# Optimization experiments

Measured on AMD Instinct MI355X. Metric: run time of the kernel, lower is better.

## Reference

```python
import jax, jax.numpy as jnp
import numpy as np
import itertools

BINS_NUM = 35
BINS_SIZE = 9
ORDERS = (2, 3, 4, 5)

def _comb_idx(n, k):
    # combinations with replacement of indices 0..n-1, shape [ncomb, k]
    return np.array(list(itertools.combinations_with_replacement(range(n), k)), dtype=np.int32)

_COMB = {k: _comb_idx(BINS_SIZE, k) for k in ORDERS}


def setup_inputs() -> dict:
    key = jax.random.key(0)
    x = jax.random.normal(key, (1024, BINS_NUM * BINS_SIZE), dtype=jnp.float32)
    return {"x": x}


def reference(x) -> jnp.ndarray:
    B = x.shape[0]
    bins = x.reshape(B, BINS_NUM, BINS_SIZE)          # [B, 35, 9]
    parts = [bins]                                     # 'origin' slice first
    for k in ORDERS:
        idx = jnp.asarray(_COMB[k])                    # [ncomb_k, k]
        gathered = bins[:, :, idx]                     # [B, 35, ncomb_k, k]
        parts.append(jnp.prod(gathered, axis=-1))      # [B, 35, ncomb_k]
    # per-bin concat [origin, de2, de3, de4, de5], then flatten bins -> matches
    # torch's outer concat over bins since bin is the leading concat axis here.
    out = jnp.concatenate(parts, axis=-1)              # [B, 35, 2001]
    return out.reshape(B, -1)                          # [B, 70035]
```

## Files before the change

### kernel.cpp

```cpp
#include <hip/hip_runtime.h>

#define BSZ 9
#define NPB 2001
#define N2 45
#define N3 165
#define N4 495
#define N5 1287
#define O2 9
#define O3 54
#define O4 219
#define O5 714
#define LSLOTS 714

#define WAVE_SYNC() asm volatile("s_waitcnt lgkmcnt(0)" ::: "memory")

constexpr unsigned pslot2(unsigned i, unsigned j) {
    return O2 + i * 9u - i * (i - 1u) / 2u + (j - i);
}

struct Tabs {
    unsigned short p2[N2];
    unsigned short p3[N3];
    unsigned short p4[N4];
    unsigned short p5[N5];
};
constexpr Tabs make_tabs() {
    Tabs t{};
    { int p = 0;
      for (unsigned i = 0; i < 9; ++i)
          for (unsigned j = i; j < 9; ++j)
              t.p2[p++] = (unsigned short)(i | (j << 8)); }
    { int p = 0;
      for (unsigned a = 0; a < 9; ++a)
          for (unsigned b = a; b < 9; ++b) {
              const unsigned ps = pslot2(a, b);
              for (unsigned c = b; c < 9; ++c)
                  t.p3[p++] = (unsigned short)(ps | (c << 8));
          } }
    { int p = 0; unsigned ts = O3;
      for (unsigned a = 0; a < 9; ++a)
          for (unsigned b = a; b < 9; ++b)
              for (unsigned c = b; c < 9; ++c) {
                  for (unsigned d = c; d < 9; ++d)
                      t.p4[p++] = (unsigned short)(ts | (d << 8));
                  ++ts;
              } }
    { int p = 0; unsigned qs = O4;
      for (unsigned a = 0; a < 9; ++a)
          for (unsigned b = a; b < 9; ++b)
              for (unsigned c = b; c < 9; ++c)
                  for (unsigned d = c; d < 9; ++d) {
                      for (unsigned e = d; e < 9; ++e)
                          t.p5[p++] = (unsigned short)(qs | (e << 10));
                      ++qs;
                  } }
    return t;
}
__constant__ Tabs g_tabs = make_tabs();

__global__ __launch_bounds__(256) void poly_expand_kernel(
        const float* __restrict__ x, float* __restrict__ out, int ntask) {
    __shared__ float L[4][LSLOTS];
    const int wave = threadIdx.x >> 6;
    const int lane = threadIdx.x & 63;
    const int task = blockIdx.x * 4 + wave;
    if (task >= ntask) return;
    float* Lw = L[wave];
    const unsigned base = (unsigned)task * NPB;

    if (lane < 9) {
        const float v = x[(size_t)task * BSZ + lane];
        Lw[lane] = v;
        out[base + lane] = v;
    }
    WAVE_SYNC();

    if (lane < N2) {
        const unsigned pk = g_tabs.p2[lane];
        const float v = Lw[pk & 255u] * Lw[pk >> 8];
        Lw[O2 + lane] = v;
        out[base + O2 + lane] = v;
    }
    WAVE_SYNC();

    #pragma unroll
    for (int k = 0; k < 3; ++k) {
        const int s = lane + 64 * k;
        if (s < N3) {
            const unsigned pk = g_tabs.p3[s];
            const float v = Lw[pk & 255u] * Lw[pk >> 8];
            Lw[O3 + s] = v;
            out[base + O3 + s] = v;
        }
    }
    WAVE_SYNC();

    #pragma unroll
    for (int k = 0; k < 8; ++k) {
        const int s = lane + 64 * k;
        if (s < N4) {
            const unsigned pk = g_tabs.p4[s];
            const float v = Lw[pk & 255u] * Lw[pk >> 8];
            Lw[O4 + s] = v;
            out[base + O4 + s] = v;
        }
    }
    WAVE_SYNC();

    #pragma unroll 4
    for (int k = 0; k < 21; ++k) {
        const int s = lane + 64 * k;
        if (s < N5) {
            const unsigned pk = g_tabs.p5[s];
            out[base + O5 + s] = Lw[pk & 1023u] * Lw[pk >> 10];
        }
    }
}

extern "C" void kernel_launch(void* const* d_in, const int* in_sizes, int n_in,
                              void* d_out, int out_size, void* d_ws, size_t ws_size,
                              hipStream_t stream) {
    const float* x = (const float*)d_in[0];
    float* out = (float*)d_out;
    const int ntask = in_sizes[0] / BSZ;
    const int blocks = (ntask + 3) / 4;
    poly_expand_kernel<<<blocks, 256, 0, stream>>>(x, out, ntask);
}
```

Before: 63.29 us.

## Defer all output writes to an aligned float4 store pass driven by a unified table

Stages now only write products into LDS. A single final pass then emits the whole 2001-float row as aligned float4 stores. Lower-order entries are copied by multiplying against a constant 1.0 slot, so one packed 32-bit table covers every output element. LDS indices get a padding swizzle (s + s>>5) to reduce bank conflicts. The aim is fewer, wider global stores in place of scalar stores at every stage, paid for with extra LDS reads, a larger constant table and head/tail handling for misaligned rows.

```diff
diff --git a/kernel.cpp b/kernel.cpp
--- a/kernel.cpp
+++ b/kernel.cpp
@@ -5,14 +5,16 @@
 #define N2 45
 #define N3 165
 #define N4 495
-#define N5 1287
 #define O2 9
 #define O3 54
 #define O4 219
-#define O5 714
-#define LSLOTS 714
+#define ONE_SLOT 714
+#define LSZ 740
 
 #define WAVE_SYNC() asm volatile("s_waitcnt lgkmcnt(0)" ::: "memory")
+
+__device__ __forceinline__ unsigned sw(unsigned s) { return s + (s >> 5); }
+constexpr unsigned csw(unsigned s) { return s + (s >> 5); }
 
 constexpr unsigned pslot2(unsigned i, unsigned j) {
     return O2 + i * 9u - i * (i - 1u) / 2u + (j - i);
@@ -22,7 +24,6 @@
     unsigned short p2[N2];
     unsigned short p3[N3];
     unsigned short p4[N4];
-    unsigned short p5[N5];
 };
 constexpr Tabs make_tabs() {
     Tabs t{};
@@ -45,41 +46,44 @@
                       t.p4[p++] = (unsigned short)(ts | (d << 8));
                   ++ts;
               } }
-    { int p = 0; unsigned qs = O4;
+    return t;
+}
+__constant__ Tabs g_tabs = make_tabs();
+
+struct Full { unsigned t[NPB]; };
+constexpr Full make_full() {
+    Full f{};
+    for (unsigned j = 0; j < ONE_SLOT; ++j)
+        f.t[j] = j | (ONE_SLOT << 16);
+    { int p = ONE_SLOT; unsigned qs = O4;
       for (unsigned a = 0; a < 9; ++a)
           for (unsigned b = a; b < 9; ++b)
               for (unsigned c = b; c < 9; ++c)
                   for (unsigned d = c; d < 9; ++d) {
                       for (unsigned e = d; e < 9; ++e)
-                          t.p5[p++] = (unsigned short)(qs | (e << 10));
+                          f.t[p++] = qs | (e << 16);
                       ++qs;
                   } }
-    return t;
+    return f;
 }
-__constant__ Tabs g_tabs = make_tabs();
+__constant__ Full g_full = make_full();
 
 __global__ __launch_bounds__(256) void poly_expand_kernel(
         const float* __restrict__ x, float* __restrict__ out, int ntask) {
-    __shared__ float L[4][LSLOTS];
+    __shared__ float L[4][LSZ];
     const int wave = threadIdx.x >> 6;
     const int lane = threadIdx.x & 63;
     const int task = blockIdx.x * 4 + wave;
     if (task >= ntask) return;
     float* Lw = L[wave];
-    const unsigned base = (unsigned)task * NPB;
 
-    if (lane < 9) {
-        const float v = x[(size_t)task * BSZ + lane];
-        Lw[lane] = v;
-        out[base + lane] = v;
-    }
+    if (lane < 9)        Lw[sw((unsigned)lane)] = x[(size_t)task * BSZ + lane];
+    else if (lane == 9)  Lw[csw(ONE_SLOT)] = 1.0f;
     WAVE_SYNC();
 
     if (lane < N2) {
         const unsigned pk = g_tabs.p2[lane];
-        const float v = Lw[pk & 255u] * Lw[pk >> 8];
-        Lw[O2 + lane] = v;
-        out[base + O2 + lane] = v;
+        Lw[sw(O2 + (unsigned)lane)] = Lw[sw(pk & 255u)] * Lw[sw(pk >> 8)];
     }
     WAVE_SYNC();
 
@@ -88,9 +92,7 @@
         const int s = lane + 64 * k;
         if (s < N3) {
             const unsigned pk = g_tabs.p3[s];
-            const float v = Lw[pk & 255u] * Lw[pk >> 8];
-            Lw[O3 + s] = v;
-            out[base + O3 + s] = v;
+            Lw[sw(O3 + (unsigned)s)] = Lw[sw(pk & 255u)] * Lw[sw(pk >> 8)];
         }
     }
     WAVE_SYNC();
@@ -100,20 +102,38 @@
         const int s = lane + 64 * k;
         if (s < N4) {
             const unsigned pk = g_tabs.p4[s];
-            const float v = Lw[pk & 255u] * Lw[pk >> 8];
-            Lw[O4 + s] = v;
-            out[base + O4 + s] = v;
+            Lw[sw(O4 + (unsigned)s)] = Lw[sw(pk & 255u)] * Lw[sw(pk >> 8)];
         }
     }
     WAVE_SYNC();
 
-    #pragma unroll 4
-    for (int k = 0; k < 21; ++k) {
-        const int s = lane + 64 * k;
-        if (s < N5) {
-            const unsigned pk = g_tabs.p5[s];
-            out[base + O5 + s] = Lw[pk & 1023u] * Lw[pk >> 10];
+    const unsigned rb = (unsigned)task * NPB;
+    const unsigned h = (unsigned)((4 - (task & 3)) & 3);
+
+    if (lane < (int)h) out[rb + lane] = Lw[sw((unsigned)lane)];
+
+    const unsigned n4 = (NPB - h) >> 2;
+    #pragma unroll 2
+    for (int k = 0; k < 8; ++k) {
+        const unsigned i = (unsigned)lane + 64u * k;
+        if (i < n4) {
+            const unsigned j0 = h + 4u * i;
+            float r[4];
+            #pragma unroll
+            for (int e = 0; e < 4; ++e) {
+                const unsigned pk = g_full.t[j0 + e];
+                r[e] = Lw[sw(pk & 0xFFFFu)] * Lw[sw(pk >> 16)];
+            }
+            *reinterpret_cast<float4*>(out + rb + j0) =
+                make_float4(r[0], r[1], r[2], r[3]);
         }
+    }
+
+    const unsigned jt = h + 4u * n4;
+    if (lane < (int)(NPB - jt)) {
+        const unsigned j = jt + (unsigned)lane;
+        const unsigned pk = g_full.t[j];
+        out[rb + j] = Lw[sw(pk & 0xFFFFu)] * Lw[sw(pk >> 16)];
     }
 }
 
```

New measurement: 61.11 us. 3.4% less time.
